# Performance work log

Measured on AMD Instinct MI355X. Metric: run time of the kernel, lower is better.

Reference implementation:

```python
import jax, jax.numpy as jnp
import numpy as np

T, J, IC = 243, 17, 32
C = J * IC            # 544 embed dim
BS = 3                # block_size
NB = T // BS          # 81 num_blocks
K = 6                 # top_k
H = 8                 # num_heads
DEPTH = 2
HID = int(C * 2.0)    # 1088 mlp hidden
EPS = 1e-6


def _ln(x, g, b):
    m = x.mean(-1, keepdims=True)
    v = ((x - m) ** 2).mean(-1, keepdims=True)
    return (x - m) * jax.lax.rsqrt(v + EPS) * g + b


def setup_inputs() -> dict:
    key = jax.random.key(0)
    ks = jax.random.split(key, 16)
    s = 0.02
    B = 512
    return {
        "x": jax.random.normal(ks[0], (B, T, J, IC), jnp.float32),
        "pos_embed": s * jax.random.normal(ks[1], (1, T, C), jnp.float32),
        "fc1_w": s * jax.random.normal(ks[2], (NB, NB), jnp.float32),
        "fc2_w": s * jax.random.normal(ks[3], (NB, NB), jnp.float32),
        "ln1_g": jnp.ones((DEPTH, C), jnp.float32),
        "ln1_b": jnp.zeros((DEPTH, C), jnp.float32),
        "qkv_w": s * jax.random.normal(ks[4], (DEPTH, 3 * C, C), jnp.float32),
        "qkv_b": jnp.zeros((DEPTH, 3 * C), jnp.float32),
        "proj_w": s * jax.random.normal(ks[5], (DEPTH, C, C), jnp.float32),
        "proj_b": jnp.zeros((DEPTH, C), jnp.float32),
        "ln2_g": jnp.ones((DEPTH, C), jnp.float32),
        "ln2_b": jnp.zeros((DEPTH, C), jnp.float32),
        "mfc1_w": s * jax.random.normal(ks[6], (DEPTH, HID, C), jnp.float32),
        "mfc1_b": jnp.zeros((DEPTH, HID), jnp.float32),
        "mfc2_w": s * jax.random.normal(ks[7], (DEPTH, C, HID), jnp.float32),
        "mfc2_b": jnp.zeros((DEPTH, C), jnp.float32),
        "lnf_g": jnp.ones((C,), jnp.float32),
        "lnf_b": jnp.zeros((C,), jnp.float32),
        "wm2_w": s * jax.random.normal(ks[8], (K,), jnp.float32),
        "wm2_b": jnp.zeros((1,), jnp.float32),
    }


def reference(x, pos_embed, fc1_w, fc2_w, ln1_g, ln1_b, qkv_w, qkv_b,
              proj_w, proj_b, ln2_g, ln2_b, mfc1_w, mfc1_b, mfc2_w, mfc2_b,
              lnf_g, lnf_b, wm2_w, wm2_b):
    B = x.shape[0]
    x = x.reshape(B, T, C) + pos_embed                       # [B,T,C]
    # time_shift: zero-pad one frame at the front, keep first T rows, first C/2 chans
    shifted = jnp.pad(x, ((0, 0), (1, 0), (0, 0)))[:, :T, :C // 2]
    x = jnp.concatenate([shifted, x[:, :, C // 2:]], axis=2)
    # block pooling
    xb = x.reshape(B, NB, BS, C).mean(axis=2)                # [B,NB,C]
    # BlockAttention: global avg over C -> gated MLP -> topk -> gather
    y = xb.mean(axis=2)                                      # [B,NB]
    y = jax.nn.sigmoid(jnp.maximum(y @ fc1_w.T, 0.0) @ fc2_w.T)
    _, idx = jax.lax.top_k(y, K)                             # [B,K]
    t = jnp.take_along_axis(xb, idx[:, :, None], axis=1)     # [B,K,C]
    scale = (C // H) ** -0.5
    for i in range(DEPTH):
        h = _ln(t, ln1_g[i], ln1_b[i])
        qkv = (h @ qkv_w[i].T + qkv_b[i]).reshape(B, K, 3, H, C // H)
        q, k, v = qkv[:, :, 0], qkv[:, :, 1], qkv[:, :, 2]   # [B,K,H,hd]
        attn = jax.nn.softmax(jnp.einsum('bnhd,bmhd->bhnm', q, k) * scale, axis=-1)
        o = jnp.einsum('bhnm,bmhd->bnhd', attn, v).reshape(B, K, C)
        t = t + o @ proj_w[i].T + proj_b[i]
        h = _ln(t, ln2_g[i], ln2_b[i])
        h = jax.nn.gelu(h @ mfc1_w[i].T + mfc1_b[i], approximate=False)
        t = t + (h @ mfc2_w[i].T + mfc2_b[i])
    t = _ln(t, lnf_g, lnf_b)
    out = jnp.einsum('bkc,k->bc', t, wm2_w) + wm2_b          # Conv1d(K,1,ks=1)
    return out.reshape(B, 1, J, C // J)
```

## Files before the change

### kernel.cpp

```cpp
#include <hip/hip_runtime.h>
#include <hip/hip_bf16.h>
#include <math.h>

#define TT 243
#define CC 544
#define NBB 81
#define KK 6
#define HH 8
#define HD 68
#define DEPTH 2
#define HID 1088
#define BB 512
#define MTOK 3072
#define EPSF 1e-6f

typedef __attribute__((ext_vector_type(8))) short bf16x8;
typedef __attribute__((ext_vector_type(4))) float f32x4;

__device__ __forceinline__ __hip_bfloat16 f2b(float f) { return __float2bfloat16(f); }
__device__ __forceinline__ unsigned short f2bu(float f) {
    __hip_bfloat16 h = __float2bfloat16(f);
    return *(unsigned short*)&h;
}
__device__ __forceinline__ float b2f_lo(unsigned int u) { return __uint_as_float(u << 16); }
__device__ __forceinline__ float b2f_hi(unsigned int u) { return __uint_as_float(u & 0xffff0000u); }

#define E0 443904
#define E1 591872
#define E2 887808
#define E3 1183744

#define RS_BLOCKS 3888
#define PS_BLOCKS 8
#define WC_BLOCKS 4624
#define BW_GRID (RS_BLOCKS + PS_BLOCKS + WC_BLOCKS)

__global__ __launch_bounds__(256, 4) void bw_kernel(
    const float* __restrict__ x,
    const float* __restrict__ pos,
    const float* __restrict__ qkvw, const float* __restrict__ projw,
    const float* __restrict__ mfc1w, const float* __restrict__ mfc2w,
    unsigned short* __restrict__ wbf,
    float* __restrict__ L,
    float* __restrict__ R,
    float* __restrict__ pLR)
{
    const int blk = blockIdx.x;
    const int tid = threadIdx.x;

    if (blk < RS_BLOCKS) {
        const int w = tid >> 6;
        const int lane = tid & 63;
        const int oct = lane & 7;
        const int rsub = lane >> 3;
        const int r = (blk * 4 + w) * 8 + rsub;
        const float4* xr = (const float4*)x + (size_t)r * 136;
        float4 xs[17];
#pragma unroll
        for (int j = 0; j < 17; ++j) xs[j] = xr[oct + j * 8];
        float aL = 0.0f, aR = 0.0f;
#pragma unroll
        for (int j = 0; j < 17; ++j) {
            const float s = (xs[j].x + xs[j].y) + (xs[j].z + xs[j].w);
            if (j < 8) aL += s;
            else if (j == 8) { if (oct < 4) aL += s; else aR += s; }
            else aR += s;
        }
#pragma unroll
        for (int m = 1; m < 8; m <<= 1) {
            aL += __shfl_xor(aL, m);
            aR += __shfl_xor(aR, m);
        }
        if (oct == 0) { L[r] = aL; R[r] = aR; }
        return;
    }

    if (blk < RS_BLOCKS + PS_BLOCKS) {
        const int w = tid >> 6;
        const int lane = tid & 63;
        const int oct = lane & 7;
        const int rsub = lane >> 3;
        const int r = (blk - RS_BLOCKS) * 32 + w * 8 + rsub;
        const int rc = (r < TT) ? r : (TT - 1);
        const float4* pr = (const float4*)pos + (size_t)rc * 136;
        float4 xs[17];
#pragma unroll
        for (int j = 0; j < 17; ++j) xs[j] = pr[oct + j * 8];
        float aL = 0.0f, aR = 0.0f;
#pragma unroll
        for (int j = 0; j < 17; ++j) {
            const float s = (xs[j].x + xs[j].y) + (xs[j].z + xs[j].w);
            if (j < 8) aL += s;
            else if (j == 8) { if (oct < 4) aL += s; else aR += s; }
            else aR += s;
        }
#pragma unroll
        for (int m = 1; m < 8; m <<= 1) {
            aL += __shfl_xor(aL, m);
            aR += __shfl_xor(aR, m);
        }
        if (oct == 0 && r < TT) { pLR[r] = aL; pLR[TT + r] = aR; }
        return;
    }

    const int i = (blk - RS_BLOCKS - PS_BLOCKS) * 256 + tid;
    if (i < E3) {
        float4 v;
        if (i < E0)      v = ((const float4*)qkvw)[i];
        else if (i < E1) v = ((const float4*)projw)[i - E0];
        else if (i < E2) v = ((const float4*)mfc1w)[i - E1];
        else             v = ((const float4*)mfc2w)[i - E2];
        ushort4 o;
        o.x = f2bu(v.x); o.y = f2bu(v.y); o.z = f2bu(v.z); o.w = f2bu(v.w);
        ((ushort4*)wbf)[i] = o;
    }
}

__global__ __launch_bounds__(128) void select_kernel(
    const float* __restrict__ L, const float* __restrict__ R,
    const float* __restrict__ pLR,
    const float* __restrict__ fc1, const float* __restrict__ fc2,
    const float* __restrict__ x, const float* __restrict__ pos,
    const float* __restrict__ ln1g, const float* __restrict__ ln1b,
    float* __restrict__ t,
    unsigned short* __restrict__ hb)
{
    const int b = blockIdx.x;
    const int tid = threadIdx.x;
    __shared__ float sf1[NBB * NBB];
    __shared__ float sf2[NBB * NBB];
    __shared__ float sy[NBB], sz[NBB], swv[NBB];
    __shared__ int sidx[KK];
    __shared__ __align__(16) float st[KK][CC];

    const int w = tid >> 6;
    const int lane = tid & 63;
    const float4* x4 = (const float4*)x;
    const float4* p4 = (const float4*)pos;

    for (int i = tid; i < NBB * NBB; i += 128) {
        sf1[i] = fc1[i];
        sf2[i] = fc2[i];
    }

    if (tid < NBB) {
        const int n = tid;
        const float* Lb = L + (size_t)b * TT;
        const float* Rb = R + (size_t)b * TT;
        const float* pL = pLR;
        const float* pR = pLR + TT;
        float s = Lb[3 * n] + Lb[3 * n + 1] + Rb[3 * n] + Rb[3 * n + 1] + Rb[3 * n + 2]
                + pL[3 * n] + pL[3 * n + 1] + pR[3 * n] + pR[3 * n + 1] + pR[3 * n + 2];
        if (n > 0) s += Lb[3 * n - 1] + pL[3 * n - 1];
        sy[n] = s * (1.0f / (3.0f * (float)CC));
    }
    __syncthreads();
    if (tid < NBB) {
        float s = 0.0f;
        for (int j = 0; j < NBB; ++j) s += sf1[tid * NBB + j] * sy[j];
        sz[tid] = fmaxf(s, 0.0f);
    }
    __syncthreads();
    if (tid < NBB) {
        float s = 0.0f;
        for (int j = 0; j < NBB; ++j) s += sf2[tid * NBB + j] * sz[j];
        swv[tid] = 1.0f / (1.0f + expf(-s));
    }
    __syncthreads();
    if (w == 0) {
        float va = (lane < NBB) ? swv[lane] : -1e30f;
        float vb = (lane + 64 < NBB) ? swv[lane + 64] : -1e30f;
        const int ia = lane, ib = lane + 64;
        for (int kk = 0; kk < KK; ++kk) {
            float v = va; int idx = ia;
            if (vb > v) { v = vb; idx = ib; }
#pragma unroll
            for (int m = 1; m < 64; m <<= 1) {
                const float ov = __shfl_xor(v, m);
                const int oi = __shfl_xor(idx, m);
                if (ov > v || (ov == v && oi < idx)) { v = ov; idx = oi; }
            }
            if (lane == 0) sidx[kk] = idx;
            if (ia == idx) va = -1e30f;
            if (ib == idx) vb = -1e30f;
        }
    }
    __syncthreads();

    for (int i = tid; i < KK * 136; i += 128) {
        const int k = i / 136;
        const int c4 = i - k * 136;
        const int n = sidx[k];
        const int shift = (c4 < 68) ? -1 : 0;
        float ax = 0.f, ay = 0.f, az = 0.f, aw = 0.f;
#pragma unroll
        for (int i2 = 0; i2 < 3; ++i2) {
            const int ttr = 3 * n + i2 + shift;
            if (ttr >= 0) {
                const float4 xv = x4[((size_t)b * TT + ttr) * 136 + c4];
                const float4 pv = p4[(size_t)ttr * 136 + c4];
                ax += xv.x + pv.x; ay += xv.y + pv.y; az += xv.z + pv.z; aw += xv.w + pv.w;
            }
        }
        const float inv3 = 1.0f / 3.0f;
        const float4 a = make_float4(ax * inv3, ay * inv3, az * inv3, aw * inv3);
        *(float4*)&st[k][c4 * 4] = a;
        ((float4*)t)[((size_t)b * KK + k) * 136 + c4] = a;
    }
    __syncthreads();

    for (int k = w; k < KK; k += 2) {
        float s = 0.0f, s2 = 0.0f;
        for (int c = lane; c < CC; c += 64) { const float v = st[k][c]; s += v; s2 += v * v; }
#pragma unroll
        for (int off = 32; off; off >>= 1) {
            s += __shfl_xor(s, off);
            s2 += __shfl_xor(s2, off);
        }
        const float m = s / (float)CC;
        const float inv = rsqrtf(s2 / (float)CC - m * m + EPSF);
        for (int c4 = lane; c4 < 136; c4 += 64) {
            const float4 v = *(const float4*)&st[k][c4 * 4];
            const float4 gv = ((const float4*)ln1g)[c4];
            const float4 bv = ((const float4*)ln1b)[c4];
            ushort4 o;
            o.x = f2bu((v.x - m) * inv * gv.x + bv.x);
            o.y = f2bu((v.y - m) * inv * gv.y + bv.y);
            o.z = f2bu((v.z - m) * inv * gv.z + bv.z);
            o.w = f2bu((v.w - m) * inv * gv.w + bv.w);
            ((ushort4*)hb)[((size_t)b * KK + k) * 136 + c4] = o;
        }
    }
}

__global__ __launch_bounds__(256) void ln_bf16_kernel(
    const float* __restrict__ X, const float* __restrict__ g,
    const float* __restrict__ bta, unsigned short* __restrict__ Y)
{
    const int row = blockIdx.x * 4 + (threadIdx.x >> 6);
    const int lane = threadIdx.x & 63;
    const float4* xr4 = (const float4*)(X + (size_t)row * CC);
    const float4 v0 = xr4[lane];
    const float4 v1 = xr4[lane + 64];
    float4 v2 = make_float4(0.f, 0.f, 0.f, 0.f);
    if (lane < 8) v2 = xr4[lane + 128];
    float s = (v0.x + v0.y + v0.z + v0.w) + (v1.x + v1.y + v1.z + v1.w)
            + (v2.x + v2.y + v2.z + v2.w);
    float s2 = (v0.x * v0.x + v0.y * v0.y + v0.z * v0.z + v0.w * v0.w)
             + (v1.x * v1.x + v1.y * v1.y + v1.z * v1.z + v1.w * v1.w)
             + (v2.x * v2.x + v2.y * v2.y + v2.z * v2.z + v2.w * v2.w);
#pragma unroll
    for (int off = 32; off; off >>= 1) {
        s += __shfl_xor(s, off);
        s2 += __shfl_xor(s2, off);
    }
    const float m = s / (float)CC;
    const float inv = rsqrtf(s2 / (float)CC - m * m + EPSF);
    ushort4* yr = (ushort4*)(Y + (size_t)row * CC);
    {
        const float4 gv = ((const float4*)g)[lane];
        const float4 bv = ((const float4*)bta)[lane];
        ushort4 o;
        o.x = f2bu((v0.x - m) * inv * gv.x + bv.x);
        o.y = f2bu((v0.y - m) * inv * gv.y + bv.y);
        o.z = f2bu((v0.z - m) * inv * gv.z + bv.z);
        o.w = f2bu((v0.w - m) * inv * gv.w + bv.w);
        yr[lane] = o;
    }
    {
        const float4 gv = ((const float4*)g)[lane + 64];
        const float4 bv = ((const float4*)bta)[lane + 64];
        ushort4 o;
        o.x = f2bu((v1.x - m) * inv * gv.x + bv.x);
        o.y = f2bu((v1.y - m) * inv * gv.y + bv.y);
        o.z = f2bu((v1.z - m) * inv * gv.z + bv.z);
        o.w = f2bu((v1.w - m) * inv * gv.w + bv.w);
        yr[lane + 64] = o;
    }
    if (lane < 8) {
        const float4 gv = ((const float4*)g)[lane + 128];
        const float4 bv = ((const float4*)bta)[lane + 128];
        ushort4 o;
        o.x = f2bu((v2.x - m) * inv * gv.x + bv.x);
        o.y = f2bu((v2.y - m) * inv * gv.y + bv.y);
        o.z = f2bu((v2.z - m) * inv * gv.z + bv.z);
        o.w = f2bu((v2.w - m) * inv * gv.w + bv.w);
        yr[lane + 128] = o;
    }
}

template <int BN, int ACT, int RES, int OBF>
__global__ __launch_bounds__(256) void gemm_mfma_kernel(
    const unsigned short* __restrict__ X,
    const unsigned short* __restrict__ W,
    const float* __restrict__ bias,
    const float* __restrict__ Rr,
    void* __restrict__ Y,
    int M, int N, int Kd)
{
    constexpr int NF = BN / 32;
    const int bm = blockIdx.y * 64;
    const int bn = blockIdx.x * BN;
    const int tid = threadIdx.x;
    const int K8 = Kd >> 3;

    __shared__ __align__(16) short As[64][72];
    __shared__ __align__(16) short Bs[BN][72];

    const int r0 = tid >> 2;
    const int c0 = tid & 3;
    const int r1 = r0 + 64;

    const uint4* Xu = (const uint4*)X;
    const uint4* Wu = (const uint4*)W;

    const int wid = tid >> 6;
    const int lane = tid & 63;
    const int wm = (wid >> 1) * 32;
    const int wn = (wid & 1) * (BN / 2);
    const int l16 = lane & 15;
    const int l4 = lane >> 4;
    const int koff = l4 * 8;

    f32x4 acc[2][NF] = {};

    const int wr0 = min(bn + r0, N - 1);
    const int wr1 = (BN == 128) ? min(bn + r1, N - 1) : 0;

    const uint4 zz = {0u, 0u, 0u, 0u};
    uint4 a00, a01, b00, b01, b10, b11;
    {
        const int k1 = c0, k2 = c0 + 4;
        a00 = (k1 < K8) ? Xu[(size_t)(bm + r0) * K8 + k1] : zz;
        a01 = (k2 < K8) ? Xu[(size_t)(bm + r0) * K8 + k2] : zz;
        b00 = (k1 < K8) ? Wu[(size_t)wr0 * K8 + k1] : zz;
        b01 = (k2 < K8) ? Wu[(size_t)wr0 * K8 + k2] : zz;
        if constexpr (BN == 128) {
            b10 = (c0 < K8) ? Wu[(size_t)wr1 * K8 + c0] : zz;
            b11 = (c0 + 4 < K8) ? Wu[(size_t)wr1 * K8 + c0 + 4] : zz;
        }
    }

    const int nk = (Kd + 63) >> 6;
    for (int kt = 0; kt < nk; ++kt) {
        __syncthreads();
        *(uint4*)&As[r0][c0 * 8]       = a00;
        *(uint4*)&As[r0][(c0 + 4) * 8] = a01;
        *(uint4*)&Bs[r0][c0 * 8]       = b00;
        *(uint4*)&Bs[r0][(c0 + 4) * 8] = b01;
        if constexpr (BN == 128) {
            *(uint4*)&Bs[r1][c0 * 8]       = b10;
            *(uint4*)&Bs[r1][(c0 + 4) * 8] = b11;
        }
        __syncthreads();

        if (kt + 1 < nk) {
            const int k1 = (kt + 1) * 8 + c0;
            const int k2 = k1 + 4;
            a00 = (k1 < K8) ? Xu[(size_t)(bm + r0) * K8 + k1] : zz;
            a01 = (k2 < K8) ? Xu[(size_t)(bm + r0) * K8 + k2] : zz;
            b00 = (k1 < K8) ? Wu[(size_t)wr0 * K8 + k1] : zz;
            b01 = (k2 < K8) ? Wu[(size_t)wr0 * K8 + k2] : zz;
            if constexpr (BN == 128) {
                b10 = (k1 < K8) ? Wu[(size_t)wr1 * K8 + k1] : zz;
                b11 = (k2 < K8) ? Wu[(size_t)wr1 * K8 + k2] : zz;
            }
        }

#pragma unroll
        for (int kh = 0; kh < 2; ++kh) {
            bf16x8 af[2], bf[NF];
#pragma unroll
            for (int mf = 0; mf < 2; ++mf)
                af[mf] = *(const bf16x8*)&As[wm + mf * 16 + l16][kh * 32 + koff];
#pragma unroll
            for (int nf = 0; nf < NF; ++nf)
                bf[nf] = *(const bf16x8*)&Bs[wn + nf * 16 + l16][kh * 32 + koff];
#pragma unroll
            for (int mf = 0; mf < 2; ++mf)
#pragma unroll
                for (int nf = 0; nf < NF; ++nf)
                    acc[mf][nf] = __builtin_amdgcn_mfma_f32_16x16x32_bf16(af[mf], bf[nf], acc[mf][nf], 0, 0, 0);
        }
    }

#pragma unroll
    for (int nf = 0; nf < NF; ++nf) {
        const int col = bn + wn + nf * 16 + l16;
        if (col < N) {
            const float bs = bias[col];
#pragma unroll
            for (int mf = 0; mf < 2; ++mf) {
#pragma unroll
                for (int j = 0; j < 4; ++j) {
                    const int row = bm + wm + mf * 16 + l4 * 4 + j;
                    float v = acc[mf][nf][j] + bs;
                    if (ACT == 1) v = 0.5f * v * (1.0f + erff(v * 0.70710678118654752f));
                    if (RES) v += Rr[(size_t)row * N + col];
                    if (OBF) ((unsigned short*)Y)[(size_t)row * N + col] = f2bu(v);
                    else     ((float*)Y)[(size_t)row * N + col] = v;
                }
            }
        }
    }
}

__global__ __launch_bounds__(512) void attn_kernel(
    const unsigned short* __restrict__ qkv,
    __hip_bfloat16* __restrict__ o)
{
    const int b = blockIdx.x;
    __shared__ __align__(16) float sq[KK * 3 * CC];
    __shared__ float sp[HH][40];
    const int tid = threadIdx.x;

    const uint4* src4 = (const uint4*)(qkv + (size_t)b * KK * 3 * CC);
    for (int i = tid; i < (KK * 3 * CC) / 8; i += 512) {
        const uint4 u = src4[i];
        float4 f0, f1;
        f0.x = b2f_lo(u.x); f0.y = b2f_hi(u.x);
        f0.z = b2f_lo(u.y); f0.w = b2f_hi(u.y);
        f1.x = b2f_lo(u.z); f1.y = b2f_hi(u.z);
        f1.z = b2f_lo(u.w); f1.w = b2f_hi(u.w);
        ((float4*)sq)[2 * i] = f0;
        ((float4*)sq)[2 * i + 1] = f1;
    }
    __syncthreads();

    const int h = tid >> 6;
    const int lane = tid & 63;
    const float scl = rsqrtf((float)HD);

    if (lane < KK * KK) {
        const int n = lane / KK, m = lane - (lane / KK) * KK;
        const float* qp = &sq[n * (3 * CC) + 0 * CC + h * HD];
        const float* kp = &sq[m * (3 * CC) + 1 * CC + h * HD];
        float s = 0.0f;
#pragma unroll 4
        for (int d = 0; d < HD; ++d) s += qp[d] * kp[d];
        sp[h][lane] = s * scl;
    }
    __syncthreads();
    if (lane < KK) {
        const int n = lane;
        float mx = -1e30f;
#pragma unroll
        for (int m = 0; m < KK; ++m) mx = fmaxf(mx, sp[h][n * KK + m]);
        float e[KK];
        float sum = 0.0f;
#pragma unroll
        for (int m = 0; m < KK; ++m) { e[m] = expf(sp[h][n * KK + m] - mx); sum += e[m]; }
        const float inv = 1.0f / sum;
#pragma unroll
        for (int m = 0; m < KK; ++m) sp[h][n * KK + m] = e[m] * inv;
    }
    __syncthreads();
    for (int i = tid; i < KK * CC; i += 512) {
        const int n = i / CC;
        const int cd = i - n * CC;
        const int hh = cd / HD;
        const int d = cd - hh * HD;
        float acc = 0.0f;
#pragma unroll
        for (int m = 0; m < KK; ++m)
            acc += sp[hh][n * KK + m] * sq[m * (3 * CC) + 2 * CC + hh * HD + d];
        o[(size_t)b * KK * CC + i] = f2b(acc);
    }
}

__global__ __launch_bounds__(256) void final_kernel(
    const float* __restrict__ t, const float* __restrict__ g,
    const float* __restrict__ bta, const float* __restrict__ wm2w,
    const float* __restrict__ wm2b, float* __restrict__ out)
{
    const int b = blockIdx.x;
    const int tid = threadIdx.x;
    __shared__ float st[KK][CC];
    __shared__ float sm[KK], si[KK];
    const float* tb = t + (size_t)b * KK * CC;
    for (int i = tid; i < KK * CC; i += 256) st[i / CC][i % CC] = tb[i];
    __syncthreads();
    const int wid = tid >> 6, lane = tid & 63;
    for (int r = wid; r < KK; r += 4) {
        float s = 0.0f, s2 = 0.0f;
        for (int c = lane; c < CC; c += 64) { const float v = st[r][c]; s += v; s2 += v * v; }
#pragma unroll
        for (int off = 32; off; off >>= 1) { s += __shfl_xor(s, off); s2 += __shfl_xor(s2, off); }
        if (lane == 0) {
            const float m = s / (float)CC;
            sm[r] = m;
            si[r] = rsqrtf(s2 / (float)CC - m * m + EPSF);
        }
    }
    __syncthreads();
    const float w0 = wm2w[0], w1 = wm2w[1], w2 = wm2w[2], w3 = wm2w[3], w4 = wm2w[4], w5 = wm2w[5];
    const float wb = wm2b[0];
    for (int c = tid; c < CC; c += 256) {
        const float gg = g[c], bb = bta[c];
        float acc = wb;
        acc += w0 * ((st[0][c] - sm[0]) * si[0] * gg + bb);
        acc += w1 * ((st[1][c] - sm[1]) * si[1] * gg + bb);
        acc += w2 * ((st[2][c] - sm[2]) * si[2] * gg + bb);
        acc += w3 * ((st[3][c] - sm[3]) * si[3] * gg + bb);
        acc += w4 * ((st[4][c] - sm[4]) * si[4] * gg + bb);
        acc += w5 * ((st[5][c] - sm[5]) * si[5] * gg + bb);
        out[(size_t)b * CC + c] = acc;
    }
}

extern "C" void kernel_launch(void* const* d_in, const int* in_sizes, int n_in,
                              void* d_out, int out_size, void* d_ws, size_t ws_size,
                              hipStream_t stream)
{
    const float* x      = (const float*)d_in[0];
    const float* pos    = (const float*)d_in[1];
    const float* fc1_w  = (const float*)d_in[2];
    const float* fc2_w  = (const float*)d_in[3];
    const float* ln1_g  = (const float*)d_in[4];
    const float* ln1_b  = (const float*)d_in[5];
    const float* qkv_w  = (const float*)d_in[6];
    const float* qkv_b  = (const float*)d_in[7];
    const float* proj_w = (const float*)d_in[8];
    const float* proj_b = (const float*)d_in[9];
    const float* ln2_g  = (const float*)d_in[10];
    const float* ln2_b  = (const float*)d_in[11];
    const float* mfc1_w = (const float*)d_in[12];
    const float* mfc1_b = (const float*)d_in[13];
    const float* mfc2_w = (const float*)d_in[14];
    const float* mfc2_b = (const float*)d_in[15];
    const float* lnf_g  = (const float*)d_in[16];
    const float* lnf_b  = (const float*)d_in[17];
    const float* wm2_w  = (const float*)d_in[18];
    const float* wm2_b  = (const float*)d_in[19];

    float* ws = (float*)d_ws;
    float* L    = ws;
    float* R    = L + 124416;
    float* pLR  = R + 124416;
    float* t    = pLR + 512;
    unsigned short* qkvb = (unsigned short*)(t + (size_t)MTOK * CC);
    unsigned short* hb  = qkvb + (size_t)MTOK * 3 * CC;
    unsigned short* ob  = hb + (size_t)MTOK * CC;
    unsigned short* gb  = ob + (size_t)MTOK * CC;
    unsigned short* wbf = gb + (size_t)MTOK * HID;

    unsigned short* wqkv = wbf;
    unsigned short* wprj = wbf + 1775616;
    unsigned short* wf1  = wbf + 2367488;
    unsigned short* wf2  = wbf + 3551232;

    bw_kernel<<<BW_GRID, 256, 0, stream>>>(
        x, pos, qkv_w, proj_w, mfc1_w, mfc2_w, wbf, L, R, pLR);

    select_kernel<<<BB, 128, 0, stream>>>(
        L, R, pLR, fc1_w, fc2_w, x, pos, ln1_g, ln1_b, t, hb);

    for (int i = 0; i < DEPTH; ++i) {
        if (i > 0) {
            ln_bf16_kernel<<<MTOK / 4, 256, 0, stream>>>(t, ln1_g + i * CC, ln1_b + i * CC, hb);
        }
        gemm_mfma_kernel<128, 0, 0, 1><<<dim3(13, 48), 256, 0, stream>>>(
            hb, wqkv + (size_t)i * 1632 * 544, qkv_b + (size_t)i * 3 * CC,
            nullptr, qkvb, MTOK, 3 * CC, CC);
        attn_kernel<<<BB, 512, 0, stream>>>(qkvb, (__hip_bfloat16*)ob);
        gemm_mfma_kernel<64, 0, 1, 0><<<dim3(9, 48), 256, 0, stream>>>(
            ob, wprj + (size_t)i * 544 * 544, proj_b + (size_t)i * CC,
            t, t, MTOK, CC, CC);
        ln_bf16_kernel<<<MTOK / 4, 256, 0, stream>>>(t, ln2_g + i * CC, ln2_b + i * CC, hb);
        gemm_mfma_kernel<128, 1, 0, 1><<<dim3(9, 48), 256, 0, stream>>>(
            hb, wf1 + (size_t)i * HID * 544, mfc1_b + (size_t)i * HID,
            nullptr, gb, MTOK, HID, CC);
        gemm_mfma_kernel<64, 0, 1, 0><<<dim3(9, 48), 256, 0, stream>>>(
            gb, wf2 + (size_t)i * 544 * HID, mfc2_b + (size_t)i * CC,
            t, t, MTOK, CC, HID);
    }

    final_kernel<<<BB, 256, 0, stream>>>(t, lnf_g, lnf_b, wm2_w, wm2_b, (float*)d_out);
}
```

Measured before the change: 228.9 us.

## Fuse attention with output projection GEMM per pair of batches

Merges the attention kernel and the projection GEMM into one kernel that handles two batches (12 tokens padded to 16 rows) per block. The attention output stays in shared memory as bf16 and feeds MFMA directly, and the residual is added in place. Q/K/V are also kept as bf16 in LDS instead of being widened to fp32. This removes one launch and the round trip of the attention output through global memory. In exchange, every block rereads the full projection weight from global or L2 and wastes a quarter of the MFMA rows on padding.

```diff
diff --git a/kernel.cpp b/kernel.cpp
--- a/kernel.cpp
+++ b/kernel.cpp
@@ -22,8 +22,9 @@
     __hip_bfloat16 h = __float2bfloat16(f);
     return *(unsigned short*)&h;
 }
-__device__ __forceinline__ float b2f_lo(unsigned int u) { return __uint_as_float(u << 16); }
-__device__ __forceinline__ float b2f_hi(unsigned int u) { return __uint_as_float(u & 0xffff0000u); }
+__device__ __forceinline__ float b2f(unsigned short u) {
+    return __uint_as_float(((unsigned)u) << 16);
+}
 
 #define E0 443904
 #define E1 591872
@@ -405,66 +406,119 @@
     }
 }
 
-__global__ __launch_bounds__(512) void attn_kernel(
+__global__ __launch_bounds__(512) void attnproj_kernel(
     const unsigned short* __restrict__ qkv,
-    __hip_bfloat16* __restrict__ o)
+    const unsigned short* __restrict__ W,
+    const float* __restrict__ bias,
+    float* __restrict__ t)
 {
-    const int b = blockIdx.x;
-    __shared__ __align__(16) float sq[KK * 3 * CC];
-    __shared__ float sp[HH][40];
+    const int b0 = blockIdx.x * 2;
     const int tid = threadIdx.x;
-
-    const uint4* src4 = (const uint4*)(qkv + (size_t)b * KK * 3 * CC);
-    for (int i = tid; i < (KK * 3 * CC) / 8; i += 512) {
-        const uint4 u = src4[i];
-        float4 f0, f1;
-        f0.x = b2f_lo(u.x); f0.y = b2f_hi(u.x);
-        f0.z = b2f_lo(u.y); f0.w = b2f_hi(u.y);
-        f1.x = b2f_lo(u.z); f1.y = b2f_hi(u.z);
-        f1.z = b2f_lo(u.w); f1.w = b2f_hi(u.w);
-        ((float4*)sq)[2 * i] = f0;
-        ((float4*)sq)[2 * i + 1] = f1;
-    }
-    __syncthreads();
-
-    const int h = tid >> 6;
+    const int w = tid >> 6;
     const int lane = tid & 63;
+
+    __shared__ __align__(16) unsigned short sqkv[2][KK * 3 * CC];
+    __shared__ __align__(16) unsigned short aolds[16][552];
+    __shared__ float sp[2][HH][40];
+
+#pragma unroll 2
+    for (int bl = 0; bl < 2; ++bl) {
+        const uint4* src = (const uint4*)(qkv + (size_t)(b0 + bl) * KK * 3 * CC);
+        uint4* dst = (uint4*)sqkv[bl];
+        for (int i = tid; i < 1224; i += 512) dst[i] = src[i];
+    }
+    __syncthreads();
+
     const float scl = rsqrtf((float)HD);
-
-    if (lane < KK * KK) {
-        const int n = lane / KK, m = lane - (lane / KK) * KK;
-        const float* qp = &sq[n * (3 * CC) + 0 * CC + h * HD];
-        const float* kp = &sq[m * (3 * CC) + 1 * CC + h * HD];
-        float s = 0.0f;
+    const int h = w;
+
+#pragma unroll 2
+    for (int bl = 0; bl < 2; ++bl) {
+        if (lane < KK * KK) {
+            const int n = lane / KK, m = lane - (lane / KK) * KK;
+            const unsigned short* qp = &sqkv[bl][n * (3 * CC) + h * HD];
+            const unsigned short* kp = &sqkv[bl][m * (3 * CC) + CC + h * HD];
+            float s = 0.0f;
 #pragma unroll 4
-        for (int d = 0; d < HD; ++d) s += qp[d] * kp[d];
-        sp[h][lane] = s * scl;
-    }
-    __syncthreads();
-    if (lane < KK) {
-        const int n = lane;
-        float mx = -1e30f;
-#pragma unroll
-        for (int m = 0; m < KK; ++m) mx = fmaxf(mx, sp[h][n * KK + m]);
-        float e[KK];
-        float sum = 0.0f;
-#pragma unroll
-        for (int m = 0; m < KK; ++m) { e[m] = expf(sp[h][n * KK + m] - mx); sum += e[m]; }
-        const float inv = 1.0f / sum;
-#pragma unroll
-        for (int m = 0; m < KK; ++m) sp[h][n * KK + m] = e[m] * inv;
-    }
-    __syncthreads();
-    for (int i = tid; i < KK * CC; i += 512) {
-        const int n = i / CC;
-        const int cd = i - n * CC;
+            for (int d = 0; d < HD; ++d) s += b2f(qp[d]) * b2f(kp[d]);
+            sp[bl][h][lane] = s * scl;
+        }
+    }
+    __syncthreads();
+#pragma unroll 2
+    for (int bl = 0; bl < 2; ++bl) {
+        if (lane < KK) {
+            const int n = lane;
+            float mx = -1e30f;
+#pragma unroll
+            for (int m = 0; m < KK; ++m) mx = fmaxf(mx, sp[bl][h][n * KK + m]);
+            float e[KK];
+            float sum = 0.0f;
+#pragma unroll
+            for (int m = 0; m < KK; ++m) { e[m] = expf(sp[bl][h][n * KK + m] - mx); sum += e[m]; }
+            const float inv = 1.0f / sum;
+#pragma unroll
+            for (int m = 0; m < KK; ++m) sp[bl][h][n * KK + m] = e[m] * inv;
+        }
+    }
+    __syncthreads();
+
+    for (int i = tid; i < 2 * KK * CC; i += 512) {
+        const int bl = i / (KK * CC);
+        const int rem = i - bl * (KK * CC);
+        const int n = rem / CC;
+        const int cd = rem - n * CC;
         const int hh = cd / HD;
         const int d = cd - hh * HD;
         float acc = 0.0f;
 #pragma unroll
         for (int m = 0; m < KK; ++m)
-            acc += sp[hh][n * KK + m] * sq[m * (3 * CC) + 2 * CC + hh * HD + d];
-        o[(size_t)b * KK * CC + i] = f2b(acc);
+            acc += sp[bl][hh][n * KK + m] * b2f(sqkv[bl][m * (3 * CC) + 2 * CC + hh * HD + d]);
+        aolds[bl * 8 + n][cd] = f2bu(acc);
+    }
+    __syncthreads();
+
+    const int l16 = lane & 15;
+    const int l4 = lane >> 4;
+    f32x4 acc[5] = {};
+
+    for (int kt = 0; kt < 17; ++kt) {
+        const int k0 = kt * 32;
+        const bf16x8 af = *(const bf16x8*)&aolds[l16][k0 + l4 * 8];
+        bf16x8 bfr[5];
+#pragma unroll
+        for (int q = 0; q < 5; ++q) {
+            const int f = w + q * 8;
+            if (f < 34) {
+                const int n0 = f * 16;
+                bfr[q] = *(const bf16x8*)&W[(size_t)(n0 + l16) * CC + k0 + l4 * 8];
+            }
+        }
+#pragma unroll
+        for (int q = 0; q < 5; ++q) {
+            const int f = w + q * 8;
+            if (f < 34)
+                acc[q] = __builtin_amdgcn_mfma_f32_16x16x32_bf16(af, bfr[q], acc[q], 0, 0, 0);
+        }
+    }
+
+#pragma unroll
+    for (int q = 0; q < 5; ++q) {
+        const int f = w + q * 8;
+        if (f < 34) {
+            const int col = f * 16 + l16;
+            const float bs = bias[col];
+#pragma unroll
+            for (int j = 0; j < 4; ++j) {
+                const int r = l4 * 4 + j;
+                const int bl = r >> 3;
+                const int n = r & 7;
+                if (n < KK) {
+                    const size_t idx = ((size_t)(b0 + bl) * KK + n) * CC + col;
+                    t[idx] = acc[q][j] + bs + t[idx];
+                }
+            }
+        }
     }
 }
 
@@ -562,10 +616,8 @@
         gemm_mfma_kernel<128, 0, 0, 1><<<dim3(13, 48), 256, 0, stream>>>(
             hb, wqkv + (size_t)i * 1632 * 544, qkv_b + (size_t)i * 3 * CC,
             nullptr, qkvb, MTOK, 3 * CC, CC);
-        attn_kernel<<<BB, 512, 0, stream>>>(qkvb, (__hip_bfloat16*)ob);
-        gemm_mfma_kernel<64, 0, 1, 0><<<dim3(9, 48), 256, 0, stream>>>(
-            ob, wprj + (size_t)i * 544 * 544, proj_b + (size_t)i * CC,
-            t, t, MTOK, CC, CC);
+        attnproj_kernel<<<BB / 2, 512, 0, stream>>>(
+            qkvb, wprj + (size_t)i * 544 * 544, proj_b + (size_t)i * CC, t);
         ln_bf16_kernel<<<MTOK / 4, 256, 0, stream>>>(t, ln2_g + i * CC, ln2_b + i * CC, hb);
         gemm_mfma_kernel<128, 1, 0, 1><<<dim3(9, 48), 256, 0, stream>>>(
             hb, wf1 + (size_t)i * HID * 544, mfc1_b + (size_t)i * HID,
```

Measured after the change: 248.2 us. 1.08x slower.
